# Optimization experiments

Measured on AMD Instinct MI355X. Metric: run time of the kernel, lower is better.

The kernel has to match this reference:

```python
import jax, jax.numpy as jnp
import numpy as np

NUM_NODE_TYPES = 16
NODE_EMBED = 128
EDGE_EMBED = 64
ATTN_DIMS = [64, 64]
EDGE_DIMS = [32, 32]
HEADS = [4, 4]
N = 50000
E = 500000


def _glorot(key, shape):
    s = jnp.sqrt(2.0 / (shape[0] + shape[1]))
    return jax.random.normal(key, shape, jnp.float32) * s


def setup_inputs() -> dict:
    key = jax.random.key(0)
    ks = jax.random.split(key, 20)
    inp = {}
    inp["node_types"] = jax.random.randint(ks[0], (N,), 0, NUM_NODE_TYPES)
    inp["src"] = jax.random.randint(ks[1], (E,), 0, N)
    inp["dst"] = jax.random.randint(ks[2], (E,), 0, N)
    inp["efeats"] = jax.random.normal(ks[3], (E, EDGE_EMBED), jnp.float32)
    inp["embed_table"] = jax.random.normal(ks[4], (NUM_NODE_TYPES, NODE_EMBED), jnp.float32)
    in_n, in_e = NODE_EMBED, EDGE_EMBED
    k = 5
    for i, (on, oe, h) in enumerate(zip(ATTN_DIMS, EDGE_DIMS, HEADS)):
        inp[f"W_src{i}"] = _glorot(ks[k], (in_n, h * on)); k += 1
        inp[f"b_src{i}"] = jnp.zeros((h * on,), jnp.float32)
        inp[f"W_ni{i}"] = _glorot(ks[k], (in_n, h * oe)); k += 1
        inp[f"W_nj{i}"] = _glorot(ks[k], (in_n, h * oe)); k += 1
        inp[f"W_fij{i}"] = _glorot(ks[k], (in_e, h * oe)); k += 1
        inp[f"attn{i}"] = _glorot(ks[k], (h, oe)); k += 1
        inp[f"bias{i}"] = jnp.zeros((h * oe,), jnp.float32)
        in_n, in_e = h * on, h * oe
    return inp


def _egat_layer(src, dst, nf, ef, W_src, b_src, W_ni, W_nj, W_fij, attn, bias, heads, oe, on):
    # per-edge feature: f_ni(src) + f_nj(dst) + f_fij(edge) + bias
    f_ni = nf @ W_ni                                   # (N, H*oe)
    f_nj = nf @ W_nj                                   # (N, H*oe)
    f_fij = ef @ W_fij                                 # (E, H*oe)
    f_out = f_ni[src] + f_nj[dst] + f_fij + bias       # (E, H*oe)
    f_out = jax.nn.leaky_relu(f_out, 0.01).reshape(-1, heads, oe)  # (E, H, oe)
    e = jnp.einsum('ehd,hd->eh', f_out, attn)          # (E, H) attention logits
    # edge_softmax over incoming edges of each dst node
    m = jax.ops.segment_max(e, dst, num_segments=N)    # (N, H)
    ee = jnp.exp(e - m[dst])
    s = jax.ops.segment_sum(ee, dst, num_segments=N)   # (N, H)
    alpha = ee / s[dst]                                # (E, H)
    h_src = (nf @ W_src + b_src).reshape(-1, heads, on)  # (N, H, on)
    msg = h_src[src] * alpha[:, :, None]               # (E, H, on)
    h_new = jax.ops.segment_sum(msg, dst, num_segments=N)  # (N, H, on)
    return h_new, f_out


def reference(node_types, src, dst, efeats, embed_table,
              W_src0, b_src0, W_ni0, W_nj0, W_fij0, attn0, bias0,
              W_src1, b_src1, W_ni1, W_nj1, W_fij1, attn1, bias1):
    nf = embed_table[node_types]                       # (N, NODE_EMBED)
    ef = efeats
    layers = [
        (W_src0, b_src0, W_ni0, W_nj0, W_fij0, attn0, bias0),
        (W_src1, b_src1, W_ni1, W_nj1, W_fij1, attn1, bias1),
    ]
    for i, p in enumerate(layers):
        h, f = _egat_layer(src, dst, nf, ef, *p, HEADS[i], EDGE_DIMS[i], ATTN_DIMS[i])
        nf = jax.nn.elu(h.reshape(N, -1))              # (N, H*on)
        ef = jax.nn.elu(f.reshape(E, -1))              # (E, H*oe)
    return nf, ef
```

## Files before the change

### kernel.cpp

```cpp
#include <hip/hip_runtime.h>
#include <hip/hip_bf16.h>

#define NN 50000
#define NE 500000

__global__ void k_embed(const int* __restrict__ nt, const float* __restrict__ table,
                        float* __restrict__ nf){
  int i = blockIdx.x * 256 + threadIdx.x;
  if (i >= NN * 128) return;
  nf[i] = table[nt[i >> 7] * 128 + (i & 127)];
}

__global__ void k_zero2(int* __restrict__ cnt, int* __restrict__ cur){
  int i = blockIdx.x * 256 + threadIdx.x;
  if (i < NN){ cnt[i] = 0; cur[i] = 0; }
}

__global__ void k_hist(const int* __restrict__ dst, int* __restrict__ cnt){
  int e = blockIdx.x * 256 + threadIdx.x;
  if (e < NE) atomicAdd(&cnt[dst[e]], 1);
}

__global__ __launch_bounds__(1024) void k_scan(const int* __restrict__ cnt,
                                               int* __restrict__ off){
  __shared__ int ws[16];
  __shared__ int blocktot;
  __shared__ int carry_s;
  int tid = threadIdx.x;
  int lane = tid & 63, wv = tid >> 6;
  if (tid == 0) carry_s = 0;
  for (int base = 0; base < NN; base += 1024){
    int i = base + tid;
    int v = (i < NN) ? cnt[i] : 0;
    int x = v;
    #pragma unroll
    for (int d = 1; d < 64; d <<= 1){
      int t = __shfl_up(x, d, 64);
      if (lane >= d) x += t;
    }
    if (lane == 63) ws[wv] = x;
    __syncthreads();
    if (tid == 0){
      int a = 0;
      #pragma unroll
      for (int k2 = 0; k2 < 16; ++k2){ int t = ws[k2]; ws[k2] = a; a += t; }
      blocktot = a;
    }
    __syncthreads();
    int carry = carry_s;
    if (i < NN) off[i] = carry + ws[wv] + (x - v);
    __syncthreads();
    if (tid == 0) carry_s = carry + blocktot;
    __syncthreads();
  }
  if (tid == 0) off[NN] = carry_s;
}

__global__ void k_scatter(const int* __restrict__ src, const int* __restrict__ dst,
                          const int* __restrict__ off, int* __restrict__ cur,
                          int* __restrict__ rank, int* __restrict__ perm_s){
  int e = blockIdx.x * 256 + threadIdx.x;
  if (e >= NE) return;
  int d = dst[e];
  int pos = off[d] + atomicAdd(&cur[d], 1);
  rank[e] = pos;
  perm_s[pos] = src[e];
}

template<int BM>
__global__ __launch_bounds__(256) void k_gemm_t(
    const float* __restrict__ A, const float* __restrict__ W,
    const float* __restrict__ bias, float* __restrict__ C,
    int M, int K, int Nc){
  constexpr int RM = BM / 16;
  constexpr int AQ = BM / 32;
  __shared__ float As[32][BM + 4];
  __shared__ float Ws[32][128];
  int tid = threadIdx.x;
  int row0 = blockIdx.x * BM;
  int col0 = blockIdx.y * 128;
  int tr = (tid >> 4) & 15;
  int tc = tid & 15;
  int wk0 = tid >> 5;
  int wcc = (tid & 31) * 4;

  float4 pa[AQ], pw[4];
  #pragma unroll
  for (int q = 0; q < AQ; ++q) pa[q] = make_float4(0.f,0.f,0.f,0.f);

  float acc[RM][8];
  #pragma unroll
  for (int i = 0; i < RM; ++i)
    #pragma unroll
    for (int j = 0; j < 8; ++j) acc[i][j] = 0.f;

  #pragma unroll
  for (int q = 0; q < AQ; ++q){
    int idx = tid + q * 256;
    int gr = row0 + (idx >> 3);
    if (gr < M) pa[q] = *reinterpret_cast<const float4*>(A + (size_t)gr * K + ((idx & 7) * 4));
  }
  #pragma unroll
  for (int q = 0; q < 4; ++q)
    pw[q] = *reinterpret_cast<const float4*>(W + (size_t)(wk0 + q * 8) * Nc + col0 + wcc);

  for (int k0 = 0; k0 < K; k0 += 32){
    #pragma unroll
    for (int q = 0; q < AQ; ++q){
      int idx = tid + q * 256;
      int r = idx >> 3, kk = (idx & 7) * 4;
      As[kk+0][r] = pa[q].x; As[kk+1][r] = pa[q].y;
      As[kk+2][r] = pa[q].z; As[kk+3][r] = pa[q].w;
    }
    #pragma unroll
    for (int q = 0; q < 4; ++q)
      *reinterpret_cast<float4*>(&Ws[wk0 + q * 8][wcc]) = pw[q];
    __syncthreads();
    if (k0 + 32 < K){
      int kn = k0 + 32;
      #pragma unroll
      for (int q = 0; q < AQ; ++q){
        int idx = tid + q * 256;
        int gr = row0 + (idx >> 3);
        pa[q] = make_float4(0.f,0.f,0.f,0.f);
        if (gr < M) pa[q] = *reinterpret_cast<const float4*>(A + (size_t)gr * K + kn + ((idx & 7) * 4));
      }
      #pragma unroll
      for (int q = 0; q < 4; ++q)
        pw[q] = *reinterpret_cast<const float4*>(W + (size_t)(kn + wk0 + q * 8) * Nc + col0 + wcc);
    }
    #pragma unroll 8
    for (int kk = 0; kk < 32; ++kk){
      float bv[8];
      float4 b0 = *reinterpret_cast<const float4*>(&Ws[kk][tc * 4]);
      float4 b1 = *reinterpret_cast<const float4*>(&Ws[kk][64 + tc * 4]);
      bv[0]=b0.x; bv[1]=b0.y; bv[2]=b0.z; bv[3]=b0.w;
      bv[4]=b1.x; bv[5]=b1.y; bv[6]=b1.z; bv[7]=b1.w;
      float av[RM];
      #pragma unroll
      for (int g = 0; g < RM / 4; ++g){
        float4 a = *reinterpret_cast<const float4*>(&As[kk][g * (BM >> 1) + tr * 4]);
        av[g*4+0]=a.x; av[g*4+1]=a.y; av[g*4+2]=a.z; av[g*4+3]=a.w;
      }
      #pragma unroll
      for (int i = 0; i < RM; ++i)
        #pragma unroll
        for (int j = 0; j < 8; ++j)
          acc[i][j] += av[i] * bv[j];
    }
    __syncthreads();
  }

  float4 bia0 = make_float4(0.f, 0.f, 0.f, 0.f), bia1 = bia0;
  if (bias){
    bia0 = *reinterpret_cast<const float4*>(bias + col0 + tc * 4);
    bia1 = *reinterpret_cast<const float4*>(bias + col0 + 64 + tc * 4);
  }
  #pragma unroll
  for (int i = 0; i < RM; ++i){
    int gr = row0 + (i >> 2) * (BM >> 1) + tr * 4 + (i & 3);
    if (gr < M){
      float4 v0 = make_float4(acc[i][0] + bia0.x, acc[i][1] + bia0.y,
                              acc[i][2] + bia0.z, acc[i][3] + bia0.w);
      float4 v1 = make_float4(acc[i][4] + bia1.x, acc[i][5] + bia1.y,
                              acc[i][6] + bia1.z, acc[i][7] + bia1.w);
      *reinterpret_cast<float4*>(C + (size_t)gr * Nc + col0 + tc * 4) = v0;
      *reinterpret_cast<float4*>(C + (size_t)gr * Nc + col0 + 64 + tc * 4) = v1;
    }
  }
}

__global__ __launch_bounds__(256) void k_gemm_edge(
    const float* __restrict__ A, const float* __restrict__ W,
    const float* __restrict__ f_ni, const float* __restrict__ f_nj,
    const float* __restrict__ bias, const float* __restrict__ attn,
    const int* __restrict__ src, const int* __restrict__ dst,
    const int* __restrict__ rank,
    float* __restrict__ ef_out, float* __restrict__ logits_csr,
    int M, int K){
  __shared__ float As[32][132];
  __shared__ float Ws[32][128];
  int tid = threadIdx.x;
  int row0 = blockIdx.x * 128;
  int tr = (tid >> 4) & 15;
  int tc = tid & 15;
  int wk0 = tid >> 5;
  int wcc = (tid & 31) * 4;

  float4 pa[4], pw[4];
  #pragma unroll
  for (int q = 0; q < 4; ++q) pa[q] = make_float4(0.f,0.f,0.f,0.f);

  float acc[8][8];
  #pragma unroll
  for (int i = 0; i < 8; ++i)
    #pragma unroll
    for (int j = 0; j < 8; ++j) acc[i][j] = 0.f;

  #pragma unroll
  for (int q = 0; q < 4; ++q){
    int idx = tid + q * 256;
    int gr = row0 + (idx >> 3);
    if (gr < M) pa[q] = *reinterpret_cast<const float4*>(A + (size_t)gr * K + ((idx & 7) * 4));
  }
  #pragma unroll
  for (int q = 0; q < 4; ++q)
    pw[q] = *reinterpret_cast<const float4*>(W + (size_t)(wk0 + q * 8) * 128 + wcc);

  for (int k0 = 0; k0 < K; k0 += 32){
    #pragma unroll
    for (int q = 0; q < 4; ++q){
      int idx = tid + q * 256;
      int r = idx >> 3, kk = (idx & 7) * 4;
      As[kk+0][r] = pa[q].x; As[kk+1][r] = pa[q].y;
      As[kk+2][r] = pa[q].z; As[kk+3][r] = pa[q].w;
    }
    #pragma unroll
    for (int q = 0; q < 4; ++q)
      *reinterpret_cast<float4*>(&Ws[wk0 + q * 8][wcc]) = pw[q];
    __syncthreads();
    if (k0 + 32 < K){
      int kn = k0 + 32;
      #pragma unroll
      for (int q = 0; q < 4; ++q){
        int idx = tid + q * 256;
        int gr = row0 + (idx >> 3);
        pa[q] = make_float4(0.f,0.f,0.f,0.f);
        if (gr < M) pa[q] = *reinterpret_cast<const float4*>(A + (size_t)gr * K + kn + ((idx & 7) * 4));
      }
      #pragma unroll
      for (int q = 0; q < 4; ++q)
        pw[q] = *reinterpret_cast<const float4*>(W + (size_t)(kn + wk0 + q * 8) * 128 + wcc);
    }
    #pragma unroll 8
    for (int kk = 0; kk < 32; ++kk){
      float bv[8];
      float4 b0 = *reinterpret_cast<const float4*>(&Ws[kk][tc * 4]);
      float4 b1 = *reinterpret_cast<const float4*>(&Ws[kk][64 + tc * 4]);
      bv[0]=b0.x; bv[1]=b0.y; bv[2]=b0.z; bv[3]=b0.w;
      bv[4]=b1.x; bv[5]=b1.y; bv[6]=b1.z; bv[7]=b1.w;
      float av[8];
      float4 a0 = *reinterpret_cast<const float4*>(&As[kk][tr * 4]);
      float4 a1 = *reinterpret_cast<const float4*>(&As[kk][64 + tr * 4]);
      av[0]=a0.x; av[1]=a0.y; av[2]=a0.z; av[3]=a0.w;
      av[4]=a1.x; av[5]=a1.y; av[6]=a1.z; av[7]=a1.w;
      #pragma unroll
      for (int i = 0; i < 8; ++i)
        #pragma unroll
        for (int j = 0; j < 8; ++j)
          acc[i][j] += av[i] * bv[j];
    }
    __syncthreads();
  }

  float4 at0 = *reinterpret_cast<const float4*>(attn + tc * 4);
  float4 at1 = *reinterpret_cast<const float4*>(attn + 64 + tc * 4);
  float4 bi0 = *reinterpret_cast<const float4*>(bias + tc * 4);
  float4 bi1 = *reinterpret_cast<const float4*>(bias + 64 + tc * 4);
  #pragma unroll
  for (int i = 0; i < 8; ++i){
    int gr = row0 + (i >> 2) * 64 + tr * 4 + (i & 3);
    if (gr >= M) continue;
    int sN = src[gr], dN = dst[gr];
    const float* ni = f_ni + (size_t)sN * 128;
    const float* nj = f_nj + (size_t)dN * 128;
    float4 n0 = *reinterpret_cast<const float4*>(ni + tc * 4);
    float4 n1 = *reinterpret_cast<const float4*>(ni + 64 + tc * 4);
    float4 m0 = *reinterpret_cast<const float4*>(nj + tc * 4);
    float4 m1 = *reinterpret_cast<const float4*>(nj + 64 + tc * 4);
    float v[8];
    v[0] = acc[i][0] + n0.x + m0.x + bi0.x;
    v[1] = acc[i][1] + n0.y + m0.y + bi0.y;
    v[2] = acc[i][2] + n0.z + m0.z + bi0.z;
    v[3] = acc[i][3] + n0.w + m0.w + bi0.w;
    v[4] = acc[i][4] + n1.x + m1.x + bi1.x;
    v[5] = acc[i][5] + n1.y + m1.y + bi1.y;
    v[6] = acc[i][6] + n1.z + m1.z + bi1.z;
    v[7] = acc[i][7] + n1.w + m1.w + bi1.w;
    #pragma unroll
    for (int j = 0; j < 8; ++j) v[j] = (v[j] >= 0.f) ? v[j] : 0.01f * v[j];
    float4 e0 = make_float4(v[0] > 0.f ? v[0] : expm1f(v[0]),
                            v[1] > 0.f ? v[1] : expm1f(v[1]),
                            v[2] > 0.f ? v[2] : expm1f(v[2]),
                            v[3] > 0.f ? v[3] : expm1f(v[3]));
    float4 e1 = make_float4(v[4] > 0.f ? v[4] : expm1f(v[4]),
                            v[5] > 0.f ? v[5] : expm1f(v[5]),
                            v[6] > 0.f ? v[6] : expm1f(v[6]),
                            v[7] > 0.f ? v[7] : expm1f(v[7]));
    *reinterpret_cast<float4*>(ef_out + (size_t)gr * 128 + tc * 4) = e0;
    *reinterpret_cast<float4*>(ef_out + (size_t)gr * 128 + 64 + tc * 4) = e1;
    float p0 = v[0]*at0.x + v[1]*at0.y + v[2]*at0.z + v[3]*at0.w;
    float p1 = v[4]*at1.x + v[5]*at1.y + v[6]*at1.z + v[7]*at1.w;
    p0 += __shfl_xor(p0, 1, 64); p0 += __shfl_xor(p0, 2, 64); p0 += __shfl_xor(p0, 4, 64);
    p1 += __shfl_xor(p1, 1, 64); p1 += __shfl_xor(p1, 2, 64); p1 += __shfl_xor(p1, 4, 64);
    float q0 = __shfl_xor(p0, 8, 64);
    float q1 = __shfl_xor(p1, 8, 64);
    if (tc == 0){
      int pos = rank[gr];
      *reinterpret_cast<float4*>(logits_csr + (size_t)pos * 4) =
          make_float4(p0, q0, p1, q1);
    }
  }
}

__global__ __launch_bounds__(256) void k_agg_csr(
    const int* __restrict__ off, const int* __restrict__ perm_s,
    const float* __restrict__ logits_csr, const float* __restrict__ h_src,
    float* __restrict__ out){
  int n = blockIdx.x;
  int c = threadIdx.x;
  int h = c >> 6;
  int beg = off[n], end = off[n + 1];
  float m = -INFINITY;
  for (int j = beg; j < end; ++j)
    m = fmaxf(m, logits_csr[(size_t)j * 4 + h]);
  float acc = 0.f, ssum = 0.f;
  int j = beg;
  for (; j + 4 <= end; j += 4){
    int s0 = perm_s[j], s1 = perm_s[j+1], s2 = perm_s[j+2], s3 = perm_s[j+3];
    float l0 = logits_csr[(size_t)j * 4 + h];
    float l1 = logits_csr[(size_t)(j+1) * 4 + h];
    float l2 = logits_csr[(size_t)(j+2) * 4 + h];
    float l3 = logits_csr[(size_t)(j+3) * 4 + h];
    float g0 = h_src[(size_t)s0 * 256 + c];
    float g1 = h_src[(size_t)s1 * 256 + c];
    float g2 = h_src[(size_t)s2 * 256 + c];
    float g3 = h_src[(size_t)s3 * 256 + c];
    float e0 = __expf(l0 - m), e1 = __expf(l1 - m);
    float e2 = __expf(l2 - m), e3 = __expf(l3 - m);
    ssum += (e0 + e1) + (e2 + e3);
    acc += e0 * g0 + e1 * g1 + e2 * g2 + e3 * g3;
  }
  for (; j < end; ++j){
    float ee = __expf(logits_csr[(size_t)j * 4 + h] - m);
    ssum += ee;
    acc += ee * h_src[(size_t)perm_s[j] * 256 + c];
  }
  float r = (end > beg) ? acc / ssum : 0.f;
  out[(size_t)n * 256 + c] = (r > 0.f) ? r : expm1f(r);
}

static void run_layer(const float* nf, int in_n, const float* ef, int in_e,
                      const float* Wsrc, const float* bsrc, const float* Wni,
                      const float* Wnj, const float* Wfij, const float* attn,
                      const float* bias, const int* src, const int* dst,
                      const int* off, const int* rank, const int* perm_s,
                      float* f_ni, float* f_nj, float* h_src, float* logits,
                      float* nf_out, float* ef_out, hipStream_t stream){
  dim3 gN((NN + 63) / 64, 1);
  dim3 gN2((NN + 63) / 64, 2);
  k_gemm_t<64><<<gN,  256, 0, stream>>>(nf, Wni, nullptr, f_ni, NN, in_n, 128);
  k_gemm_t<64><<<gN,  256, 0, stream>>>(nf, Wnj, nullptr, f_nj, NN, in_n, 128);
  k_gemm_t<64><<<gN2, 256, 0, stream>>>(nf, Wsrc, bsrc, h_src, NN, in_n, 256);
  k_gemm_edge<<<(NE + 127) / 128, 256, 0, stream>>>(
      ef, Wfij, f_ni, f_nj, bias, attn, src, dst, rank, ef_out, logits, NE, in_e);
  k_agg_csr<<<NN, 256, 0, stream>>>(off, perm_s, logits, h_src, nf_out);
}

extern "C" void kernel_launch(void* const* d_in, const int* in_sizes, int n_in,
                              void* d_out, int out_size, void* d_ws, size_t ws_size,
                              hipStream_t stream){
  const int*   node_types = (const int*)d_in[0];
  const int*   src        = (const int*)d_in[1];
  const int*   dst        = (const int*)d_in[2];
  const float* efeats     = (const float*)d_in[3];
  const float* table      = (const float*)d_in[4];
  const float* W_src0 = (const float*)d_in[5];
  const float* b_src0 = (const float*)d_in[6];
  const float* W_ni0  = (const float*)d_in[7];
  const float* W_nj0  = (const float*)d_in[8];
  const float* W_fij0 = (const float*)d_in[9];
  const float* attn0  = (const float*)d_in[10];
  const float* bias0  = (const float*)d_in[11];
  const float* W_src1 = (const float*)d_in[12];
  const float* b_src1 = (const float*)d_in[13];
  const float* W_ni1  = (const float*)d_in[14];
  const float* W_nj1  = (const float*)d_in[15];
  const float* W_fij1 = (const float*)d_in[16];
  const float* attn1  = (const float*)d_in[17];
  const float* bias1  = (const float*)d_in[18];

  char* w = (char*)d_ws;
  auto alloc = [&](size_t bytes){ void* p = (void*)w; w += (bytes + 255) & ~(size_t)255; return p; };
  float* nf_buf = (float*)alloc((size_t)NN * 256 * 4);
  float* f_ni   = (float*)alloc((size_t)NN * 128 * 4);
  float* f_nj   = (float*)alloc((size_t)NN * 128 * 4);
  float* h_src  = (float*)alloc((size_t)NN * 256 * 4);
  float* logits = (float*)alloc((size_t)NE * 4 * 4);
  int*   cnt    = (int*)  alloc((size_t)NN * 4);
  int*   cur    = (int*)  alloc((size_t)NN * 4);
  int*   off    = (int*)  alloc((size_t)(NN + 1) * 4);
  int*   rank   = (int*)  alloc((size_t)NE * 4);
  int*   perm_s = (int*)  alloc((size_t)NE * 4);

  float* out_nf = (float*)d_out;
  float* out_ef = out_nf + (size_t)NN * 256;

  k_zero2<<<(NN + 255)/256, 256, 0, stream>>>(cnt, cur);
  k_hist<<<(NE + 255)/256, 256, 0, stream>>>(dst, cnt);
  k_scan<<<1, 1024, 0, stream>>>(cnt, off);
  k_scatter<<<(NE + 255)/256, 256, 0, stream>>>(src, dst, off, cur, rank, perm_s);

  k_embed<<<(NN*128)/256, 256, 0, stream>>>(node_types, table, nf_buf);

  run_layer(nf_buf, 128, efeats, 64,
            W_src0, b_src0, W_ni0, W_nj0, W_fij0, attn0, bias0,
            src, dst, off, rank, perm_s,
            f_ni, f_nj, h_src, logits, nf_buf, out_ef, stream);

  run_layer(nf_buf, 256, out_ef, 128,
            W_src1, b_src1, W_ni1, W_nj1, W_fij1, attn1, bias1,
            src, dst, off, rank, perm_s,
            f_ni, f_nj, h_src, logits, out_nf, out_ef, stream);
}
```

Baseline: 1.644 ms.

## Vectorize embed and aggregation with float4, drop register prefetch in edge GEMM

The embedding gather now copies float4 elements, and the CSR aggregation kernel assigns one wavefront per node instead of one block, with each lane gathering a float4 of the source features. The edge GEMM loses its register-staged prefetch of the next K tile and loads global data straight into shared memory each iteration. The aggregation change targets wasted threads and scalar gathers. Removing the prefetch lowers register pressure but exposes global load latency in the GEMM.

```diff
diff --git a/kernel.cpp b/kernel.cpp
--- a/kernel.cpp
+++ b/kernel.cpp
@@ -7,8 +7,9 @@
 __global__ void k_embed(const int* __restrict__ nt, const float* __restrict__ table,
                         float* __restrict__ nf){
   int i = blockIdx.x * 256 + threadIdx.x;
-  if (i >= NN * 128) return;
-  nf[i] = table[nt[i >> 7] * 128 + (i & 127)];
+  if (i >= NN * 32) return;
+  const float4* t4 = reinterpret_cast<const float4*>(table);
+  reinterpret_cast<float4*>(nf)[i] = t4[nt[i >> 5] * 32 + (i & 31)];
 }
 
 __global__ void k_zero2(int* __restrict__ cnt, int* __restrict__ cur){
@@ -184,66 +185,41 @@
   int row0 = blockIdx.x * 128;
   int tr = (tid >> 4) & 15;
   int tc = tid & 15;
-  int wk0 = tid >> 5;
-  int wcc = (tid & 31) * 4;
-
-  float4 pa[4], pw[4];
-  #pragma unroll
-  for (int q = 0; q < 4; ++q) pa[q] = make_float4(0.f,0.f,0.f,0.f);
 
   float acc[8][8];
   #pragma unroll
   for (int i = 0; i < 8; ++i)
     #pragma unroll
     for (int j = 0; j < 8; ++j) acc[i][j] = 0.f;
-
-  #pragma unroll
-  for (int q = 0; q < 4; ++q){
-    int idx = tid + q * 256;
-    int gr = row0 + (idx >> 3);
-    if (gr < M) pa[q] = *reinterpret_cast<const float4*>(A + (size_t)gr * K + ((idx & 7) * 4));
-  }
-  #pragma unroll
-  for (int q = 0; q < 4; ++q)
-    pw[q] = *reinterpret_cast<const float4*>(W + (size_t)(wk0 + q * 8) * 128 + wcc);
 
   for (int k0 = 0; k0 < K; k0 += 32){
     #pragma unroll
     for (int q = 0; q < 4; ++q){
       int idx = tid + q * 256;
-      int r = idx >> 3, kk = (idx & 7) * 4;
-      As[kk+0][r] = pa[q].x; As[kk+1][r] = pa[q].y;
-      As[kk+2][r] = pa[q].z; As[kk+3][r] = pa[q].w;
-    }
-    #pragma unroll
-    for (int q = 0; q < 4; ++q)
-      *reinterpret_cast<float4*>(&Ws[wk0 + q * 8][wcc]) = pw[q];
-    __syncthreads();
-    if (k0 + 32 < K){
-      int kn = k0 + 32;
-      #pragma unroll
-      for (int q = 0; q < 4; ++q){
-        int idx = tid + q * 256;
-        int gr = row0 + (idx >> 3);
-        pa[q] = make_float4(0.f,0.f,0.f,0.f);
-        if (gr < M) pa[q] = *reinterpret_cast<const float4*>(A + (size_t)gr * K + kn + ((idx & 7) * 4));
-      }
-      #pragma unroll
-      for (int q = 0; q < 4; ++q)
-        pw[q] = *reinterpret_cast<const float4*>(W + (size_t)(kn + wk0 + q * 8) * 128 + wcc);
-    }
+      int r  = idx >> 3;
+      int kk = (idx & 7) * 4;
+      float4 v = make_float4(0.f, 0.f, 0.f, 0.f);
+      int gr = row0 + r;
+      if (gr < M) v = *reinterpret_cast<const float4*>(A + (size_t)gr * K + k0 + ((idx & 7) * 4));
+      As[kk+0][r] = v.x; As[kk+1][r] = v.y; As[kk+2][r] = v.z; As[kk+3][r] = v.w;
+    }
+    #pragma unroll
+    for (int q = 0; q < 4; ++q){
+      int idx = tid + q * 256;
+      int kk = idx >> 5;
+      int cc = (idx & 31) * 4;
+      *reinterpret_cast<float4*>(&Ws[kk][cc]) =
+          *reinterpret_cast<const float4*>(W + (size_t)(k0 + kk) * 128 + cc);
+    }
+    __syncthreads();
     #pragma unroll 8
     for (int kk = 0; kk < 32; ++kk){
-      float bv[8];
+      float4 a0 = *reinterpret_cast<const float4*>(&As[kk][tr * 4]);
+      float4 a1 = *reinterpret_cast<const float4*>(&As[kk][64 + tr * 4]);
       float4 b0 = *reinterpret_cast<const float4*>(&Ws[kk][tc * 4]);
       float4 b1 = *reinterpret_cast<const float4*>(&Ws[kk][64 + tc * 4]);
-      bv[0]=b0.x; bv[1]=b0.y; bv[2]=b0.z; bv[3]=b0.w;
-      bv[4]=b1.x; bv[5]=b1.y; bv[6]=b1.z; bv[7]=b1.w;
-      float av[8];
-      float4 a0 = *reinterpret_cast<const float4*>(&As[kk][tr * 4]);
-      float4 a1 = *reinterpret_cast<const float4*>(&As[kk][64 + tr * 4]);
-      av[0]=a0.x; av[1]=a0.y; av[2]=a0.z; av[3]=a0.w;
-      av[4]=a1.x; av[5]=a1.y; av[6]=a1.z; av[7]=a1.w;
+      float av[8] = {a0.x, a0.y, a0.z, a0.w, a1.x, a1.y, a1.z, a1.w};
+      float bv[8] = {b0.x, b0.y, b0.z, b0.w, b1.x, b1.y, b1.z, b1.w};
       #pragma unroll
       for (int i = 0; i < 8; ++i)
         #pragma unroll
@@ -307,14 +283,16 @@
     const int* __restrict__ off, const int* __restrict__ perm_s,
     const float* __restrict__ logits_csr, const float* __restrict__ h_src,
     float* __restrict__ out){
-  int n = blockIdx.x;
-  int c = threadIdx.x;
-  int h = c >> 6;
+  int n = blockIdx.x * 4 + (threadIdx.x >> 6);
+  if (n >= NN) return;
+  int lane = threadIdx.x & 63;
+  int h = lane >> 4;
   int beg = off[n], end = off[n + 1];
   float m = -INFINITY;
   for (int j = beg; j < end; ++j)
     m = fmaxf(m, logits_csr[(size_t)j * 4 + h]);
-  float acc = 0.f, ssum = 0.f;
+  float4 acc = make_float4(0.f, 0.f, 0.f, 0.f);
+  float ssum = 0.f;
   int j = beg;
   for (; j + 4 <= end; j += 4){
     int s0 = perm_s[j], s1 = perm_s[j+1], s2 = perm_s[j+2], s3 = perm_s[j+3];
@@ -322,22 +300,31 @@
     float l1 = logits_csr[(size_t)(j+1) * 4 + h];
     float l2 = logits_csr[(size_t)(j+2) * 4 + h];
     float l3 = logits_csr[(size_t)(j+3) * 4 + h];
-    float g0 = h_src[(size_t)s0 * 256 + c];
-    float g1 = h_src[(size_t)s1 * 256 + c];
-    float g2 = h_src[(size_t)s2 * 256 + c];
-    float g3 = h_src[(size_t)s3 * 256 + c];
+    float4 g0 = *reinterpret_cast<const float4*>(h_src + (size_t)s0 * 256 + lane * 4);
+    float4 g1 = *reinterpret_cast<const float4*>(h_src + (size_t)s1 * 256 + lane * 4);
+    float4 g2 = *reinterpret_cast<const float4*>(h_src + (size_t)s2 * 256 + lane * 4);
+    float4 g3 = *reinterpret_cast<const float4*>(h_src + (size_t)s3 * 256 + lane * 4);
     float e0 = __expf(l0 - m), e1 = __expf(l1 - m);
     float e2 = __expf(l2 - m), e3 = __expf(l3 - m);
     ssum += (e0 + e1) + (e2 + e3);
-    acc += e0 * g0 + e1 * g1 + e2 * g2 + e3 * g3;
+    acc.x += e0*g0.x + e1*g1.x + e2*g2.x + e3*g3.x;
+    acc.y += e0*g0.y + e1*g1.y + e2*g2.y + e3*g3.y;
+    acc.z += e0*g0.z + e1*g1.z + e2*g2.z + e3*g3.z;
+    acc.w += e0*g0.w + e1*g1.w + e2*g2.w + e3*g3.w;
   }
   for (; j < end; ++j){
     float ee = __expf(logits_csr[(size_t)j * 4 + h] - m);
+    float4 g = *reinterpret_cast<const float4*>(h_src + (size_t)perm_s[j] * 256 + lane * 4);
     ssum += ee;
-    acc += ee * h_src[(size_t)perm_s[j] * 256 + c];
-  }
-  float r = (end > beg) ? acc / ssum : 0.f;
-  out[(size_t)n * 256 + c] = (r > 0.f) ? r : expm1f(r);
+    acc.x += ee * g.x; acc.y += ee * g.y; acc.z += ee * g.z; acc.w += ee * g.w;
+  }
+  float inv = (end > beg) ? 1.f / ssum : 0.f;
+  float r0 = acc.x * inv, r1 = acc.y * inv, r2 = acc.z * inv, r3 = acc.w * inv;
+  float4 o = make_float4(r0 > 0.f ? r0 : expm1f(r0),
+                         r1 > 0.f ? r1 : expm1f(r1),
+                         r2 > 0.f ? r2 : expm1f(r2),
+                         r3 > 0.f ? r3 : expm1f(r3));
+  *reinterpret_cast<float4*>(out + (size_t)n * 256 + lane * 4) = o;
 }
 
 static void run_layer(const float* nf, int in_n, const float* ef, int in_e,
@@ -354,7 +341,7 @@
   k_gemm_t<64><<<gN2, 256, 0, stream>>>(nf, Wsrc, bsrc, h_src, NN, in_n, 256);
   k_gemm_edge<<<(NE + 127) / 128, 256, 0, stream>>>(
       ef, Wfij, f_ni, f_nj, bias, attn, src, dst, rank, ef_out, logits, NE, in_e);
-  k_agg_csr<<<NN, 256, 0, stream>>>(off, perm_s, logits, h_src, nf_out);
+  k_agg_csr<<<(NN + 3) / 4, 256, 0, stream>>>(off, perm_s, logits, h_src, nf_out);
 }
 
 extern "C" void kernel_launch(void* const* d_in, const int* in_sizes, int n_in,
@@ -401,7 +388,7 @@
   k_scan<<<1, 1024, 0, stream>>>(cnt, off);
   k_scatter<<<(NE + 255)/256, 256, 0, stream>>>(src, dst, off, cur, rank, perm_s);
 
-  k_embed<<<(NN*128)/256, 256, 0, stream>>>(node_types, table, nf_buf);
+  k_embed<<<(NN*32 + 255)/256, 256, 0, stream>>>(node_types, table, nf_buf);
 
   run_layer(nf_buf, 128, efeats, 64,
             W_src0, b_src0, W_ni0, W_nj0, W_fij0, attn0, bias0,
```

Measured after the change: 1.417 ms. 1.16x faster.
